# Kernel tuning notes

Hardware: AMD Instinct MI355X
Metric: run time of the kernel (lower is better)

The kernel has to match this reference:

```python
import jax, jax.numpy as jnp
import numpy as np
import math

N = 100000          # nodes
E = 3200000         # edges
F_IN = 500          # num_features
HID = 64            # hidden
C = 64              # num_classes
K = 5               # trig frequencies
OMEGA = 1.0
D = 10              # Taylor order / diffusion hops


def _taylor_coeffs():
    # cos/sin Taylor coefficient tables, [K, D+1] (static, fp64 then cast)
    x = (np.arange(1, K + 1) * OMEGA * np.pi)[:, None].astype(np.float64)
    cosc = np.zeros((K, D + 1), np.float64)
    sinc = np.zeros((K, D + 1), np.float64)
    even = np.arange(0, D + 1, 2)
    cosc[:, ::2] = ((-1.0) ** (even // 2)) * x ** even / np.array([math.factorial(int(o)) for o in even], np.float64)
    odd = np.arange(1, D + 1, 2)
    sinc[:, 1::2] = ((-1.0) ** ((odd - 1) // 2)) * x ** odd / np.array([math.factorial(int(o)) for o in odd], np.float64)
    return jnp.asarray(sinc, jnp.float32), jnp.asarray(cosc, jnp.float32)

SINC, COSC = _taylor_coeffs()


def setup_inputs() -> dict:
    key = jax.random.key(0)
    ks = jax.random.split(key, 8)
    feature = jax.random.normal(ks[0], (N, F_IN), dtype=jnp.float32)
    edges = jax.random.randint(ks[1], (2, E), 0, N, dtype=jnp.int64)
    W1 = jax.random.normal(ks[2], (F_IN, HID), dtype=jnp.float32) * (1.0 / np.sqrt(F_IN))
    b1 = jnp.zeros((HID,), jnp.float32)
    W2 = jax.random.normal(ks[3], (HID, C), dtype=jnp.float32) * (1.0 / np.sqrt(HID))
    b2 = jnp.zeros((C,), jnp.float32)
    xav = np.sqrt(2.0 / (1 + K))  # xavier_normal for (1, K)
    alpha = jax.random.normal(ks[4], (1, K), dtype=jnp.float32) * xav
    beta = jax.random.normal(ks[5], (1, K), dtype=jnp.float32) * xav
    return {"feature": feature, "edges": edges, "W1": W1, "b1": b1,
            "W2": W2, "b2": b2, "alpha": alpha, "beta": beta}


def reference(feature, edges, W1, b1, W2, b2, alpha, beta):
    # dropout is identity in eval mode
    x = jnp.maximum(feature @ W1 + b1, 0.0)   # lin1 + relu
    x = x @ W2 + b2                           # lin2 -> [N, C]

    # ---- Trigo_prop.__norm__: sym-normalized Laplacian, rescale, self-loops -1 ----
    src, dst = edges[0], edges[1]
    not_loop = src != dst                     # remove_self_loops
    deg = jax.ops.segment_sum(jnp.where(not_loop, 1.0, 0.0).astype(x.dtype), src, num_segments=N)
    dinv = jnp.where(deg > 0, jax.lax.rsqrt(deg), 0.0)
    w_off = jnp.where(not_loop, -(dinv[src] * dinv[dst]), 0.0)   # off-diag of L_sym
    # Laplacian diagonal entries are all 1 -> lambda_max = 2*max(all weights)
    lam = 2.0 * jnp.maximum(jnp.max(w_off), 1.0)
    s = 2.0 / lam
    w_off = w_off * s
    diag = s * 1.0 - 1.0                      # scaled diag(1) plus appended -1 self-loop

    # ---- D-hop Taylor-weighted diffusion ----
    coeff = (alpha @ SINC + beta @ COSC)[0]   # [D+1]
    Tx = x
    hidden = coeff[0] * Tx
    for d in range(1, D + 1):                 # fixed small D, unrolled
        Tx = jax.ops.segment_sum(w_off[:, None] * Tx[src], dst, num_segments=N) + diag * Tx
        hidden = hidden + coeff[d] * Tx
    out = hidden + x
    return jax.nn.log_softmax(out, axis=1)
```

## Files before the change

kernel.cpp:

```cpp
#include <hip/hip_runtime.h>
#include <math.h>

#define NN 100000
#define FIN 500
#define HIDN 64
#define KF 5
#define DORD 10
#define KPAD 512
#define NKT 8

typedef unsigned short ushort_t;
typedef __attribute__((ext_vector_type(8))) short short8v;
typedef __attribute__((ext_vector_type(4))) float f32x4;

struct Tables { float sinc[KF][DORD+1]; float cosc[KF][DORD+1]; };

__device__ inline float bl(unsigned u) { return __uint_as_float(u << 16); }
__device__ inline float bh(unsigned u) { return __uint_as_float(u & 0xffff0000u); }
__device__ inline unsigned short bf16_rne(float x) {
    unsigned u = __float_as_uint(x);
    return (unsigned short)((u + 0x7fffu + ((u >> 16) & 1u)) >> 16);
}
__device__ inline unsigned pack_bf16x2(float a, float b) {
    return (unsigned)bf16_rne(a) | ((unsigned)bf16_rne(b) << 16);
}

__global__ void coeff_kernel(const float* __restrict__ alpha, const float* __restrict__ beta,
                             Tables tb, float* __restrict__ coeff) {
    int d = threadIdx.x;
    if (d <= DORD) {
        float c = 0.f;
        #pragma unroll
        for (int k = 0; k < KF; ++k)
            c += alpha[k] * tb.sinc[k][d] + beta[k] * tb.cosc[k][d];
        coeff[d] = c;
    }
}

#define CHUNK 4096

__global__ __launch_bounds__(256) void hist_kernel(
    const int* __restrict__ src, const int* __restrict__ dst,
    int* __restrict__ histD, int* __restrict__ histS, int E, int nb) {
    __shared__ int hD[512];
    __shared__ int hS[512];
    for (int i = threadIdx.x; i < 512; i += 256) { hD[i] = 0; hS[i] = 0; }
    __syncthreads();
    int base = blockIdx.x * CHUNK;
    int end = base + CHUNK; if (end > E) end = E;
    for (int e = base + threadIdx.x; e < end; e += 256) {
        int s = src[e], d = dst[e];
        if (s != d) {
            atomicAdd(&hD[d >> 8], 1);
            atomicAdd(&hS[s >> 8], 1);
        }
    }
    __syncthreads();
    size_t ro = (size_t)blockIdx.x * 512;
    for (int i = threadIdx.x; i < nb; i += 256) {
        histD[ro + i] = hD[i];
        histS[ro + i] = hS[i];
    }
}

__global__ __launch_bounds__(512) void scanA_kernel(
    int* __restrict__ histD, int* __restrict__ histS,
    int* __restrict__ totD, int* __restrict__ totS, int nchunk, int nb) {
    __shared__ int tmp[512];
    int x = blockIdx.x;
    int* hist; int* tot; int b;
    if (x < nb) { hist = histD; tot = totD; b = x; }
    else        { hist = histS; tot = totS; b = x - nb; }
    int t = threadIdx.x;
    int carry = 0;
    for (int c0 = 0; c0 < nchunk; c0 += 512) {
        int c = c0 + t;
        tmp[t] = (c < nchunk) ? hist[(size_t)c * 512 + b] : 0;
        __syncthreads();
        for (int off = 1; off < 512; off <<= 1) {
            int add = (t >= off) ? tmp[t - off] : 0;
            __syncthreads();
            tmp[t] += add;
            __syncthreads();
        }
        if (c < nchunk) hist[(size_t)c * 512 + b] = carry + ((t > 0) ? tmp[t - 1] : 0);
        carry += tmp[511];
        __syncthreads();
    }
    if (t == 0) tot[b] = carry;
}

__global__ __launch_bounds__(512) void scanB_kernel(
    const int* __restrict__ totD, const int* __restrict__ totS,
    int* __restrict__ offD, int* __restrict__ offS, int nb) {
    __shared__ int tmp[512];
    int t = threadIdx.x;
    tmp[t] = (t < nb) ? totD[t] : 0;
    __syncthreads();
    for (int off = 1; off < 512; off <<= 1) {
        int add = (t >= off) ? tmp[t - off] : 0;
        __syncthreads();
        tmp[t] += add;
        __syncthreads();
    }
    if (t < nb) offD[t] = (t > 0) ? tmp[t - 1] : 0;
    if (t == nb - 1) offD[nb] = tmp[t];
    __syncthreads();
    tmp[t] = (t < nb) ? totS[t] : 0;
    __syncthreads();
    for (int off = 1; off < 512; off <<= 1) {
        int add = (t >= off) ? tmp[t - off] : 0;
        __syncthreads();
        tmp[t] += add;
        __syncthreads();
    }
    if (t < nb) offS[t] = (t > 0) ? tmp[t - 1] : 0;
    if (t == nb - 1) offS[nb] = tmp[t];
}

__global__ __launch_bounds__(256) void scatter_kernel(
    const int* __restrict__ src, const int* __restrict__ dst,
    const int* __restrict__ histD, const int* __restrict__ histS,
    const int* __restrict__ offD, const int* __restrict__ offS,
    unsigned* __restrict__ binned, unsigned char* __restrict__ srcbin, int E, int nb) {
    __shared__ int cD[512];
    __shared__ int cS[512];
    size_t ro = (size_t)blockIdx.x * 512;
    for (int i = threadIdx.x; i < nb; i += 256) {
        cD[i] = offD[i] + histD[ro + i];
        cS[i] = offS[i] + histS[ro + i];
    }
    __syncthreads();
    int base = blockIdx.x * CHUNK;
    int end = base + CHUNK; if (end > E) end = E;
    for (int e = base + threadIdx.x; e < end; e += 256) {
        int s = src[e], d = dst[e];
        if (s != d) {
            int pD = atomicAdd(&cD[d >> 8], 1);
            binned[pD] = (unsigned)s | ((unsigned)(d & 255) << 24);
            int pS = atomicAdd(&cS[s >> 8], 1);
            srcbin[pS] = (unsigned char)(s & 255);
        }
    }
}

__global__ __launch_bounds__(256) void bucket_csr_kernel(
    const unsigned* __restrict__ binned, const int* __restrict__ offD,
    int* __restrict__ row_ptr, int* __restrict__ col, int n, int nb) {
    int b = blockIdx.x;
    int e0 = offD[b], e1 = offD[b + 1];
    int d0 = b << 8;
    int dn = n - d0; if (dn > 256) dn = 256;
    __shared__ int ind[256];
    __shared__ int cur[256];
    int t = threadIdx.x;
    ind[t] = 0;
    __syncthreads();
    for (int e = e0 + t; e < e1; e += 256) {
        unsigned p = binned[e];
        atomicAdd(&ind[p >> 24], 1);
    }
    __syncthreads();
    for (int off = 1; off < 256; off <<= 1) {
        int add = (t >= off) ? ind[t - off] : 0;
        __syncthreads();
        ind[t] += add;
        __syncthreads();
    }
    if (t < dn) {
        int excl = (t > 0) ? ind[t - 1] : 0;
        row_ptr[d0 + t] = e0 + excl;
        cur[t] = e0 + excl;
    }
    if (b == 0 && t == 0) row_ptr[n] = offD[nb];
    __syncthreads();
    for (int e = e0 + t; e < e1; e += 256) {
        unsigned p = binned[e];
        int pos = atomicAdd(&cur[p >> 24], 1);
        col[pos] = (int)(p & 0xFFFFFFu);
    }
}

__global__ __launch_bounds__(256) void dinv_count_kernel(
    const unsigned char* __restrict__ srcbin, const int* __restrict__ offS,
    float* __restrict__ dinv, int n, int nb) {
    __shared__ int ind[256];
    int b = blockIdx.x;
    int t = threadIdx.x;
    ind[t] = 0;
    __syncthreads();
    int e0 = offS[b], e1 = offS[b + 1];
    for (int e = e0 + t; e < e1; e += 256)
        atomicAdd(&ind[srcbin[e]], 1);
    __syncthreads();
    int i = (b << 8) + t;
    if (i < n) {
        int c = ind[t];
        dinv[i] = (c > 0) ? (1.0f / sqrtf((float)c)) : 0.f;
    }
}

__global__ __launch_bounds__(256) void wprep_kernel(
    const float* __restrict__ W1, ushort_t* __restrict__ Wt) {
    int tid = blockIdx.x * 256 + threadIdx.x;
    if (tid >= 64 * KPAD) return;
    int kk = tid & (KPAD - 1);
    int c = tid >> 9;
    float v = (kk < FIN) ? W1[(size_t)kk * 64 + c] : 0.f;
    Wt[(size_t)c * KPAD + kk] = bf16_rne(v);
}

__global__ __launch_bounds__(256) void gemm1_mfma_kernel(
    const float* __restrict__ A, const ushort_t* __restrict__ Wt,
    const float* __restrict__ bias, float* __restrict__ H, int n) {
    __shared__ ushort_t sA[128][72];
    __shared__ ushort_t sB[64][72];
    int t = threadIdx.x;
    int w = t >> 6;
    int lane = t & 63;
    int lr = lane & 15;
    int lg = lane >> 4;
    int rowBase = blockIdx.x * 128;

    f32x4 acc[2][4];
    #pragma unroll
    for (int r = 0; r < 2; ++r)
        #pragma unroll
        for (int c = 0; c < 4; ++c)
            acc[r][c] = (f32x4){0.f, 0.f, 0.f, 0.f};

    for (int kt = 0; kt < NKT; ++kt) {
        #pragma unroll
        for (int l = 0; l < 8; ++l) {
            int idx = t + l * 256;
            int r = idx >> 4;
            int kc = (idx & 15) * 4;
            int gr = rowBase + r;
            int gk = kt * 64 + kc;
            float4 v = make_float4(0.f, 0.f, 0.f, 0.f);
            if (gr < n) {
                if (gk + 3 < FIN) {
                    v = *(const float4*)(A + (size_t)gr * FIN + gk);
                } else {
                    float* vp = (float*)&v;
                    #pragma unroll
                    for (int j = 0; j < 4; ++j)
                        if (gk + j < FIN) vp[j] = A[(size_t)gr * FIN + gk + j];
                }
            }
            uint2 p;
            p.x = pack_bf16x2(v.x, v.y);
            p.y = pack_bf16x2(v.z, v.w);
            *(uint2*)&sA[r][kc] = p;
        }
        #pragma unroll
        for (int l = 0; l < 2; ++l) {
            int idx = t + l * 256;
            int c = idx >> 3;
            int kc = (idx & 7) * 8;
            uint4 v = *(const uint4*)(Wt + (size_t)c * KPAD + kt * 64 + kc);
            *(uint4*)&sB[c][kc] = v;
        }
        __syncthreads();

        short8v af[2][2], bfr[4][2];
        #pragma unroll
        for (int r = 0; r < 2; ++r)
            #pragma unroll
            for (int h = 0; h < 2; ++h)
                af[r][h] = *(const short8v*)&sA[w * 32 + r * 16 + lr][h * 32 + lg * 8];
        #pragma unroll
        for (int c = 0; c < 4; ++c)
            #pragma unroll
            for (int h = 0; h < 2; ++h)
                bfr[c][h] = *(const short8v*)&sB[c * 16 + lr][h * 32 + lg * 8];
        #pragma unroll
        for (int r = 0; r < 2; ++r)
            #pragma unroll
            for (int c = 0; c < 4; ++c)
                #pragma unroll
                for (int h = 0; h < 2; ++h)
                    acc[r][c] = __builtin_amdgcn_mfma_f32_16x16x32_bf16(
                        af[r][h], bfr[c][h], acc[r][c], 0, 0, 0);
        __syncthreads();
    }

    float bcol[4];
    #pragma unroll
    for (int c = 0; c < 4; ++c) bcol[c] = bias[c * 16 + lr];
    #pragma unroll
    for (int r = 0; r < 2; ++r) {
        #pragma unroll
        for (int c = 0; c < 4; ++c) {
            #pragma unroll
            for (int i = 0; i < 4; ++i) {
                int row = rowBase + w * 32 + r * 16 + lg * 4 + i;
                if (row < n)
                    H[(size_t)row * 64 + c * 16 + lr] = fmaxf(acc[r][c][i] + bcol[c], 0.f);
            }
        }
    }
}

__global__ __launch_bounds__(256) void gemm2_kernel(
    const float* __restrict__ H, const float* __restrict__ W2,
    const float* __restrict__ b2, const float* __restrict__ coeff,
    const float* __restrict__ dinv, ushort_t* __restrict__ ty0,
    float* __restrict__ out, int n) {
    __shared__ float sW[64 * 64];
    __shared__ float sb[64];
    int t = threadIdx.x;
    for (int i = t; i < 4096; i += 256) sW[i] = W2[i];
    if (t < 64) sb[t] = b2[t];
    __syncthreads();
    float c0p1 = 1.f + coeff[0];
    int lane = t & 63;
    int wid = t >> 6;
    int r0 = blockIdx.x * 128;
    int rend = r0 + 128; if (rend > n) rend = n;
    for (int r = r0 + wid; r < rend; r += 4) {
        float hv = H[(size_t)r * 64 + lane];
        float dr = dinv[r];
        float acc = sb[lane];
        #pragma unroll
        for (int k = 0; k < 64; ++k)
            acc = fmaf(__shfl(hv, k, 64), sW[k * 64 + lane], acc);
        ty0[(size_t)r * 64 + lane] = bf16_rne(dr * acc);
        out[(size_t)r * 64 + lane] = c0p1 * acc;
    }
}

__global__ __launch_bounds__(256) void spmm_kernel(
    const int* __restrict__ row_ptr, const int* __restrict__ col,
    const float* __restrict__ dinv, const ushort_t* __restrict__ tyin,
    ushort_t* __restrict__ tyout, float* __restrict__ out,
    const float* __restrict__ coeff, int d, int n, int fuse_lsm) {
    int wave = (blockIdx.x * blockDim.x + threadIdx.x) >> 6;
    if (wave >= n) return;
    int lane = threadIdx.x & 63;
    int sub = lane >> 3;
    int fl = lane & 7;
    int e0 = row_ptr[wave], e1 = row_ptr[wave + 1];
    float a0 = 0.f, a1 = 0.f, a2 = 0.f, a3 = 0.f;
    float a4 = 0.f, a5 = 0.f, a6 = 0.f, a7 = 0.f;
    int e = e0 + sub;
    for (; e + 8 < e1; e += 16) {
        int s0 = col[e], s1 = col[e + 8];
        uint4 p0 = *(const uint4*)(tyin + (size_t)s0 * 64 + fl * 8);
        uint4 p1 = *(const uint4*)(tyin + (size_t)s1 * 64 + fl * 8);
        a0 += bl(p0.x) + bl(p1.x); a1 += bh(p0.x) + bh(p1.x);
        a2 += bl(p0.y) + bl(p1.y); a3 += bh(p0.y) + bh(p1.y);
        a4 += bl(p0.z) + bl(p1.z); a5 += bh(p0.z) + bh(p1.z);
        a6 += bl(p0.w) + bl(p1.w); a7 += bh(p0.w) + bh(p1.w);
    }
    if (e < e1) {
        int s = col[e];
        uint4 p = *(const uint4*)(tyin + (size_t)s * 64 + fl * 8);
        a0 += bl(p.x); a1 += bh(p.x); a2 += bl(p.y); a3 += bh(p.y);
        a4 += bl(p.z); a5 += bh(p.z); a6 += bl(p.w); a7 += bh(p.w);
    }
    #pragma unroll
    for (int off = 8; off <= 32; off <<= 1) {
        a0 += __shfl_xor(a0, off, 64); a1 += __shfl_xor(a1, off, 64);
        a2 += __shfl_xor(a2, off, 64); a3 += __shfl_xor(a3, off, 64);
        a4 += __shfl_xor(a4, off, 64); a5 += __shfl_xor(a5, off, 64);
        a6 += __shfl_xor(a6, off, 64); a7 += __shfl_xor(a7, off, 64);
    }
    float dr = dinv[wave];
    float cd = coeff[d];
    float t0 = -dr * a0, t1 = -dr * a1, t2 = -dr * a2, t3 = -dr * a3;
    float t4 = -dr * a4, t5 = -dr * a5, t6 = -dr * a6, t7 = -dr * a7;
    if (!fuse_lsm) {
        if (sub == 0) {
            float4 o0 = *(const float4*)(out + (size_t)wave * 64 + fl * 8);
            float4 o1 = *(const float4*)(out + (size_t)wave * 64 + fl * 8 + 4);
            o0.x += cd * t0; o0.y += cd * t1; o0.z += cd * t2; o0.w += cd * t3;
            o1.x += cd * t4; o1.y += cd * t5; o1.z += cd * t6; o1.w += cd * t7;
            *(float4*)(out + (size_t)wave * 64 + fl * 8) = o0;
            *(float4*)(out + (size_t)wave * 64 + fl * 8 + 4) = o1;
            uint4 ty;
            ty.x = pack_bf16x2(dr * t0, dr * t1);
            ty.y = pack_bf16x2(dr * t2, dr * t3);
            ty.z = pack_bf16x2(dr * t4, dr * t5);
            ty.w = pack_bf16x2(dr * t6, dr * t7);
            *(uint4*)(tyout + (size_t)wave * 64 + fl * 8) = ty;
        }
    } else {
        float4 o0 = *(const float4*)(out + (size_t)wave * 64 + fl * 8);
        float4 o1 = *(const float4*)(out + (size_t)wave * 64 + fl * 8 + 4);
        o0.x += cd * t0; o0.y += cd * t1; o0.z += cd * t2; o0.w += cd * t3;
        o1.x += cd * t4; o1.y += cd * t5; o1.z += cd * t6; o1.w += cd * t7;
        float m = fmaxf(fmaxf(fmaxf(o0.x, o0.y), fmaxf(o0.z, o0.w)),
                        fmaxf(fmaxf(o1.x, o1.y), fmaxf(o1.z, o1.w)));
        #pragma unroll
        for (int off = 1; off < 8; off <<= 1) m = fmaxf(m, __shfl_xor(m, off, 64));
        float se = expf(o0.x - m) + expf(o0.y - m) + expf(o0.z - m) + expf(o0.w - m)
                 + expf(o1.x - m) + expf(o1.y - m) + expf(o1.z - m) + expf(o1.w - m);
        #pragma unroll
        for (int off = 1; off < 8; off <<= 1) se += __shfl_xor(se, off, 64);
        float lse = m + logf(se);
        o0.x -= lse; o0.y -= lse; o0.z -= lse; o0.w -= lse;
        o1.x -= lse; o1.y -= lse; o1.z -= lse; o1.w -= lse;
        if (sub == 0) {
            *(float4*)(out + (size_t)wave * 64 + fl * 8) = o0;
            *(float4*)(out + (size_t)wave * 64 + fl * 8 + 4) = o1;
        }
    }
}

extern "C" void kernel_launch(void* const* d_in, const int* in_sizes, int n_in,
                              void* d_out, int out_size, void* d_ws, size_t ws_size,
                              hipStream_t stream) {
    const float* feature = (const float*)d_in[0];
    const int*   edges   = (const int*)d_in[1];
    const float* W1      = (const float*)d_in[2];
    const float* b1      = (const float*)d_in[3];
    const float* W2      = (const float*)d_in[4];
    const float* b2      = (const float*)d_in[5];
    const float* alpha   = (const float*)d_in[6];
    const float* beta    = (const float*)d_in[7];
    float* out = (float*)d_out;

    const int n = in_sizes[0] / FIN;
    const int E = in_sizes[1] / 2;
    const int* src = edges;
    const int* dst = edges + E;

    const int nb = (n + 255) >> 8;
    const int nchunk = (E + CHUNK - 1) / CHUNK;
    const size_t n64 = (size_t)n * 64;

    char* ws = (char*)d_ws;
    size_t off = 0;
    auto alloc = [&](size_t bytes) { size_t o = off; off = (off + bytes + 255) & ~(size_t)255; return o; };
    float*         coeff   = (float*)        (ws + alloc(64 * 4));
    float*         dinv    = (float*)        (ws + alloc((size_t)n * 4));
    int*           row_ptr = (int*)          (ws + alloc(((size_t)n + 1) * 4));
    int*           offD    = (int*)          (ws + alloc(513 * 4));
    int*           offS    = (int*)          (ws + alloc(513 * 4));
    int*           totD    = (int*)          (ws + alloc(512 * 4));
    int*           totS    = (int*)          (ws + alloc(512 * 4));
    ushort_t*      Wt      = (ushort_t*)     (ws + alloc((size_t)64 * KPAD * 2));
    int*           histD   = (int*)          (ws + alloc((size_t)nchunk * 512 * 4));
    int*           histS   = (int*)          (ws + alloc((size_t)nchunk * 512 * 4));
    int*           col     = (int*)          (ws + alloc((size_t)E * 4));
    unsigned*      binned  = (unsigned*)     (ws + alloc((size_t)E * 4));
    unsigned char* srcbin  = (unsigned char*)(ws + alloc((size_t)E));
    float*         H       = (float*)        (ws + alloc(n64 * 4));
    ushort_t*      TyA     = (ushort_t*)     (ws + alloc(n64 * 2));
    ushort_t*      TyB     = (ushort_t*)     (ws + alloc(n64 * 2));

    Tables tb;
    for (int k = 0; k < KF; ++k) {
        double x = M_PI * (double)(k + 1);
        double p = 1.0, f = 1.0;
        for (int o = 0; o <= DORD; ++o) {
            if (o > 0) { p *= x; f *= (double)o; }
            double v = p / f;
            tb.cosc[k][o] = (o % 2 == 0) ? (float)((((o / 2) % 2 == 0) ? 1.0 : -1.0) * v) : 0.f;
            tb.sinc[k][o] = (o % 2 == 1) ? (float)(((((o - 1) / 2) % 2 == 0) ? 1.0 : -1.0) * v) : 0.f;
        }
    }

    coeff_kernel<<<1, 64, 0, stream>>>(alpha, beta, tb, coeff);
    wprep_kernel<<<(64 * KPAD + 255) / 256, 256, 0, stream>>>(W1, Wt);

    hist_kernel<<<nchunk, 256, 0, stream>>>(src, dst, histD, histS, E, nb);
    scanA_kernel<<<2 * nb, 512, 0, stream>>>(histD, histS, totD, totS, nchunk, nb);
    scanB_kernel<<<1, 512, 0, stream>>>(totD, totS, offD, offS, nb);
    scatter_kernel<<<nchunk, 256, 0, stream>>>(src, dst, histD, histS, offD, offS,
                                               binned, srcbin, E, nb);
    bucket_csr_kernel<<<nb, 256, 0, stream>>>(binned, offD, row_ptr, col, n, nb);
    dinv_count_kernel<<<nb, 256, 0, stream>>>(srcbin, offS, dinv, n, nb);

    gemm1_mfma_kernel<<<(n + 127) / 128, 256, 0, stream>>>(feature, Wt, b1, H, n);
    gemm2_kernel<<<(n + 127) / 128, 256, 0, stream>>>(H, W2, b2, coeff, dinv, TyA, out, n);

    const ushort_t* tin = TyA;
    ushort_t* bufs[2] = { TyB, TyA };
    for (int d = 1; d <= DORD; ++d) {
        ushort_t* tout = bufs[(d - 1) & 1];
        spmm_kernel<<<(n + 3) / 4, 256, 0, stream>>>(row_ptr, col, dinv, tin, tout, out,
                                                     coeff, d, n, d == DORD ? 1 : 0);
        tin = tout;
    }
}
```

Before: 1.181 ms.

## Fuse ten SpMM diffusion hops into one persistent kernel with grid barriers

Replaces the ten per-hop SpMM launches with a single persistent kernel of 1536 blocks. Each wave owns a fixed range of rows and keeps their output accumulators in shared memory across hops, with hops separated by a software grid barrier built on atomics. This removes launch gaps and the per-hop read-modify-write of the fp32 output in global memory. In exchange it relies on all blocks being co-resident to avoid deadlock, and it loses dynamic load balancing because each wave processes up to 17 rows serially. If 17 × 6144 waves were fewer than n, rows would be silently skipped, though that does not happen for n=100000.

```diff
diff --git a/kernel.cpp b/kernel.cpp
--- a/kernel.cpp
+++ b/kernel.cpp
@@ -8,6 +8,8 @@
 #define DORD 10
 #define KPAD 512
 #define NKT 8
+#define FUSE_GRID 1536
+#define RPW_MAX 17
 
 typedef unsigned short ushort_t;
 typedef __attribute__((ext_vector_type(8))) short short8v;
@@ -330,81 +332,104 @@
     }
 }
 
-__global__ __launch_bounds__(256) void spmm_kernel(
+__device__ __forceinline__ void grid_bar(int* cnt, int* flag, int nblk) {
+    __syncthreads();
+    if (threadIdx.x == 0) {
+        __threadfence();
+        int old = __hip_atomic_fetch_add(cnt, 1, __ATOMIC_ACQ_REL, __HIP_MEMORY_SCOPE_AGENT);
+        if (old == nblk - 1) {
+            __hip_atomic_store(flag, 1, __ATOMIC_RELEASE, __HIP_MEMORY_SCOPE_AGENT);
+        } else {
+            while (__hip_atomic_load(flag, __ATOMIC_RELAXED, __HIP_MEMORY_SCOPE_AGENT) == 0)
+                __builtin_amdgcn_s_sleep(8);
+        }
+        __threadfence();
+    }
+    __syncthreads();
+}
+
+__global__ __launch_bounds__(256, 6) void diffuse_kernel(
     const int* __restrict__ row_ptr, const int* __restrict__ col,
-    const float* __restrict__ dinv, const ushort_t* __restrict__ tyin,
-    ushort_t* __restrict__ tyout, float* __restrict__ out,
-    const float* __restrict__ coeff, int d, int n, int fuse_lsm) {
-    int wave = (blockIdx.x * blockDim.x + threadIdx.x) >> 6;
-    if (wave >= n) return;
-    int lane = threadIdx.x & 63;
+    const float* __restrict__ dinv, const float* __restrict__ coeff,
+    ushort_t* TyA, ushort_t* TyB,
+    float* out, int* bars, int n) {
+    __shared__ float oacc[4][RPW_MAX][64];
+    int t = threadIdx.x;
+    int w = t >> 6, lane = t & 63;
     int sub = lane >> 3;
     int fl = lane & 7;
-    int e0 = row_ptr[wave], e1 = row_ptr[wave + 1];
-    float a0 = 0.f, a1 = 0.f, a2 = 0.f, a3 = 0.f;
-    float a4 = 0.f, a5 = 0.f, a6 = 0.f, a7 = 0.f;
-    int e = e0 + sub;
-    for (; e + 8 < e1; e += 16) {
-        int s0 = col[e], s1 = col[e + 8];
-        uint4 p0 = *(const uint4*)(tyin + (size_t)s0 * 64 + fl * 8);
-        uint4 p1 = *(const uint4*)(tyin + (size_t)s1 * 64 + fl * 8);
-        a0 += bl(p0.x) + bl(p1.x); a1 += bh(p0.x) + bh(p1.x);
-        a2 += bl(p0.y) + bl(p1.y); a3 += bh(p0.y) + bh(p1.y);
-        a4 += bl(p0.z) + bl(p1.z); a5 += bh(p0.z) + bh(p1.z);
-        a6 += bl(p0.w) + bl(p1.w); a7 += bh(p0.w) + bh(p1.w);
-    }
-    if (e < e1) {
-        int s = col[e];
-        uint4 p = *(const uint4*)(tyin + (size_t)s * 64 + fl * 8);
-        a0 += bl(p.x); a1 += bh(p.x); a2 += bl(p.y); a3 += bh(p.y);
-        a4 += bl(p.z); a5 += bh(p.z); a6 += bl(p.w); a7 += bh(p.w);
-    }
-    #pragma unroll
-    for (int off = 8; off <= 32; off <<= 1) {
-        a0 += __shfl_xor(a0, off, 64); a1 += __shfl_xor(a1, off, 64);
-        a2 += __shfl_xor(a2, off, 64); a3 += __shfl_xor(a3, off, 64);
-        a4 += __shfl_xor(a4, off, 64); a5 += __shfl_xor(a5, off, 64);
-        a6 += __shfl_xor(a6, off, 64); a7 += __shfl_xor(a7, off, 64);
-    }
-    float dr = dinv[wave];
-    float cd = coeff[d];
-    float t0 = -dr * a0, t1 = -dr * a1, t2 = -dr * a2, t3 = -dr * a3;
-    float t4 = -dr * a4, t5 = -dr * a5, t6 = -dr * a6, t7 = -dr * a7;
-    if (!fuse_lsm) {
-        if (sub == 0) {
-            float4 o0 = *(const float4*)(out + (size_t)wave * 64 + fl * 8);
-            float4 o1 = *(const float4*)(out + (size_t)wave * 64 + fl * 8 + 4);
-            o0.x += cd * t0; o0.y += cd * t1; o0.z += cd * t2; o0.w += cd * t3;
-            o1.x += cd * t4; o1.y += cd * t5; o1.z += cd * t6; o1.w += cd * t7;
-            *(float4*)(out + (size_t)wave * 64 + fl * 8) = o0;
-            *(float4*)(out + (size_t)wave * 64 + fl * 8 + 4) = o1;
-            uint4 ty;
-            ty.x = pack_bf16x2(dr * t0, dr * t1);
-            ty.y = pack_bf16x2(dr * t2, dr * t3);
-            ty.z = pack_bf16x2(dr * t4, dr * t5);
-            ty.w = pack_bf16x2(dr * t6, dr * t7);
-            *(uint4*)(tyout + (size_t)wave * 64 + fl * 8) = ty;
-        }
-    } else {
-        float4 o0 = *(const float4*)(out + (size_t)wave * 64 + fl * 8);
-        float4 o1 = *(const float4*)(out + (size_t)wave * 64 + fl * 8 + 4);
-        o0.x += cd * t0; o0.y += cd * t1; o0.z += cd * t2; o0.w += cd * t3;
-        o1.x += cd * t4; o1.y += cd * t5; o1.z += cd * t6; o1.w += cd * t7;
-        float m = fmaxf(fmaxf(fmaxf(o0.x, o0.y), fmaxf(o0.z, o0.w)),
-                        fmaxf(fmaxf(o1.x, o1.y), fmaxf(o1.z, o1.w)));
-        #pragma unroll
-        for (int off = 1; off < 8; off <<= 1) m = fmaxf(m, __shfl_xor(m, off, 64));
-        float se = expf(o0.x - m) + expf(o0.y - m) + expf(o0.z - m) + expf(o0.w - m)
-                 + expf(o1.x - m) + expf(o1.y - m) + expf(o1.z - m) + expf(o1.w - m);
-        #pragma unroll
-        for (int off = 1; off < 8; off <<= 1) se += __shfl_xor(se, off, 64);
-        float lse = m + logf(se);
-        o0.x -= lse; o0.y -= lse; o0.z -= lse; o0.w -= lse;
-        o1.x -= lse; o1.y -= lse; o1.z -= lse; o1.w -= lse;
-        if (sub == 0) {
-            *(float4*)(out + (size_t)wave * 64 + fl * 8) = o0;
-            *(float4*)(out + (size_t)wave * 64 + fl * 8 + 4) = o1;
-        }
+    int nblk = gridDim.x;
+    int nw = nblk * 4;
+    int rpw = (n + nw - 1) / nw;
+    if (rpw > RPW_MAX) rpw = RPW_MAX;
+    int gid = blockIdx.x * 4 + w;
+    int r0 = gid * rpw;
+    int r1 = r0 + rpw; if (r1 > n) r1 = n;
+    int fmap = fl * 8 + sub;
+
+    for (int r = r0; r < r1; ++r)
+        oacc[w][r - r0][lane] = out[(size_t)r * 64 + fmap];
+
+    for (int d = 1; d <= DORD; ++d) {
+        const ushort_t* tin = ((d - 1) & 1) ? TyB : TyA;
+        ushort_t* tout = (d & 1) ? TyB : TyA;
+        float cd = coeff[d];
+        for (int r = r0; r < r1; ++r) {
+            int e0 = row_ptr[r], e1 = row_ptr[r + 1];
+            float a0 = 0.f, a1 = 0.f, a2 = 0.f, a3 = 0.f;
+            float a4 = 0.f, a5 = 0.f, a6 = 0.f, a7 = 0.f;
+            int e = e0 + sub;
+            for (; e + 8 < e1; e += 16) {
+                int s0 = col[e], s1 = col[e + 8];
+                uint4 p0 = *(const uint4*)(tin + (size_t)s0 * 64 + fl * 8);
+                uint4 p1 = *(const uint4*)(tin + (size_t)s1 * 64 + fl * 8);
+                a0 += bl(p0.x) + bl(p1.x); a1 += bh(p0.x) + bh(p1.x);
+                a2 += bl(p0.y) + bl(p1.y); a3 += bh(p0.y) + bh(p1.y);
+                a4 += bl(p0.z) + bl(p1.z); a5 += bh(p0.z) + bh(p1.z);
+                a6 += bl(p0.w) + bl(p1.w); a7 += bh(p0.w) + bh(p1.w);
+            }
+            if (e < e1) {
+                int s = col[e];
+                uint4 p = *(const uint4*)(tin + (size_t)s * 64 + fl * 8);
+                a0 += bl(p.x); a1 += bh(p.x); a2 += bl(p.y); a3 += bh(p.y);
+                a4 += bl(p.z); a5 += bh(p.z); a6 += bl(p.w); a7 += bh(p.w);
+            }
+            #pragma unroll
+            for (int off = 8; off <= 32; off <<= 1) {
+                a0 += __shfl_xor(a0, off, 64); a1 += __shfl_xor(a1, off, 64);
+                a2 += __shfl_xor(a2, off, 64); a3 += __shfl_xor(a3, off, 64);
+                a4 += __shfl_xor(a4, off, 64); a5 += __shfl_xor(a5, off, 64);
+                a6 += __shfl_xor(a6, off, 64); a7 += __shfl_xor(a7, off, 64);
+            }
+            float dr = dinv[r];
+            float t0 = -dr * a0, t1 = -dr * a1, t2 = -dr * a2, t3 = -dr * a3;
+            float t4 = -dr * a4, t5 = -dr * a5, t6 = -dr * a6, t7 = -dr * a7;
+            if (d < DORD && sub == 0) {
+                uint4 ty;
+                ty.x = pack_bf16x2(dr * t0, dr * t1);
+                ty.y = pack_bf16x2(dr * t2, dr * t3);
+                ty.z = pack_bf16x2(dr * t4, dr * t5);
+                ty.w = pack_bf16x2(dr * t6, dr * t7);
+                *(uint4*)(tout + (size_t)r * 64 + fl * 8) = ty;
+            }
+            float tj = (sub < 4) ? ((sub < 2) ? (sub == 0 ? t0 : t1) : (sub == 2 ? t2 : t3))
+                                 : ((sub < 6) ? (sub == 4 ? t4 : t5) : (sub == 6 ? t6 : t7));
+            oacc[w][r - r0][lane] += cd * tj;
+        }
+        if (d < DORD)
+            grid_bar(&bars[2 * d], &bars[2 * d + 1], nblk);
+    }
+
+    for (int r = r0; r < r1; ++r) {
+        float v = oacc[w][r - r0][lane];
+        float m = v;
+        #pragma unroll
+        for (int off = 1; off < 64; off <<= 1) m = fmaxf(m, __shfl_xor(m, off, 64));
+        float s = expf(v - m);
+        #pragma unroll
+        for (int off = 1; off < 64; off <<= 1) s += __shfl_xor(s, off, 64);
+        float lse = m + logf(s);
+        out[(size_t)r * 64 + fmap] = v - lse;
     }
 }
 
@@ -434,6 +459,7 @@
     size_t off = 0;
     auto alloc = [&](size_t bytes) { size_t o = off; off = (off + bytes + 255) & ~(size_t)255; return o; };
     float*         coeff   = (float*)        (ws + alloc(64 * 4));
+    int*           bars    = (int*)          (ws + alloc(64 * 4));
     float*         dinv    = (float*)        (ws + alloc((size_t)n * 4));
     int*           row_ptr = (int*)          (ws + alloc(((size_t)n + 1) * 4));
     int*           offD    = (int*)          (ws + alloc(513 * 4));
@@ -462,6 +488,7 @@
         }
     }
 
+    hipMemsetAsync(bars, 0, 64 * 4, stream);
     coeff_kernel<<<1, 64, 0, stream>>>(alpha, beta, tb, coeff);
     wprep_kernel<<<(64 * KPAD + 255) / 256, 256, 0, stream>>>(W1, Wt);
 
@@ -476,12 +503,6 @@
     gemm1_mfma_kernel<<<(n + 127) / 128, 256, 0, stream>>>(feature, Wt, b1, H, n);
     gemm2_kernel<<<(n + 127) / 128, 256, 0, stream>>>(H, W2, b2, coeff, dinv, TyA, out, n);
 
-    const ushort_t* tin = TyA;
-    ushort_t* bufs[2] = { TyB, TyA };
-    for (int d = 1; d <= DORD; ++d) {
-        ushort_t* tout = bufs[(d - 1) & 1];
-        spmm_kernel<<<(n + 3) / 4, 256, 0, stream>>>(row_ptr, col, dinv, tin, tout, out,
-                                                     coeff, d, n, d == DORD ? 1 : 0);
-        tin = tout;
-    }
-}
+    diffuse_kernel<<<FUSE_GRID, 256, 0, stream>>>(row_ptr, col, dinv, coeff,
+                                                  TyA, TyB, out, bars, n);
+}
```

After: 3.483 ms. +194.9%, slower.

## Fuse second linear layer into MFMA GEMM1 and unroll SpMM gather by four

Applied to the files above, without the earlier changes.

Fuses the lin2 matmul into the first MFMA GEMM kernel. The ReLU hidden tile is written to shared memory as bf16, then multiplied by a pre-transposed bf16 W2 with MFMA. This removes the fp32 H intermediate round trip through global memory and one kernel launch. Separately, the SpMM gather loop gets a four-edge unrolled stage so more loads are in flight. The tradeoff is bf16 rounding of the hidden activations before lin2, plus extra LDS use.

```diff
diff --git a/kernel.cpp b/kernel.cpp
--- a/kernel.cpp
+++ b/kernel.cpp
@@ -201,26 +201,45 @@
 }
 
 __global__ __launch_bounds__(256) void wprep_kernel(
-    const float* __restrict__ W1, ushort_t* __restrict__ Wt) {
+    const float* __restrict__ W1, const float* __restrict__ W2,
+    ushort_t* __restrict__ Wt, ushort_t* __restrict__ W2t) {
     int tid = blockIdx.x * 256 + threadIdx.x;
-    if (tid >= 64 * KPAD) return;
-    int kk = tid & (KPAD - 1);
-    int c = tid >> 9;
-    float v = (kk < FIN) ? W1[(size_t)kk * 64 + c] : 0.f;
-    Wt[(size_t)c * KPAD + kk] = bf16_rne(v);
-}
-
-__global__ __launch_bounds__(256) void gemm1_mfma_kernel(
+    if (tid < 64 * KPAD) {
+        int kk = tid & (KPAD - 1);
+        int c = tid >> 9;
+        float v = (kk < FIN) ? W1[(size_t)kk * 64 + c] : 0.f;
+        Wt[(size_t)c * KPAD + kk] = bf16_rne(v);
+    } else if (tid < 64 * KPAD + 64 * 64) {
+        int j = tid - 64 * KPAD;
+        int kk = j & 63;
+        int c = j >> 6;
+        W2t[(size_t)c * 64 + kk] = bf16_rne(W2[(size_t)kk * 64 + c]);
+    }
+}
+
+__global__ __launch_bounds__(256) void gemm12_kernel(
     const float* __restrict__ A, const ushort_t* __restrict__ Wt,
-    const float* __restrict__ bias, float* __restrict__ H, int n) {
+    const ushort_t* __restrict__ W2t,
+    const float* __restrict__ b1, const float* __restrict__ b2,
+    const float* __restrict__ coeff, const float* __restrict__ dinv,
+    ushort_t* __restrict__ ty0, float* __restrict__ out, int n) {
     __shared__ ushort_t sA[128][72];
     __shared__ ushort_t sB[64][72];
+    __shared__ ushort_t sB2[64][72];
     int t = threadIdx.x;
     int w = t >> 6;
     int lane = t & 63;
     int lr = lane & 15;
     int lg = lane >> 4;
     int rowBase = blockIdx.x * 128;
+
+    #pragma unroll
+    for (int l = 0; l < 2; ++l) {
+        int idx = t + l * 256;
+        int c = idx >> 3, kc = (idx & 7) * 8;
+        uint4 v = *(const uint4*)(W2t + (size_t)c * 64 + kc);
+        *(uint4*)&sB2[c][kc] = v;
+    }
 
     f32x4 acc[2][4];
     #pragma unroll
@@ -285,48 +304,64 @@
         __syncthreads();
     }
 
-    float bcol[4];
-    #pragma unroll
-    for (int c = 0; c < 4; ++c) bcol[c] = bias[c * 16 + lr];
+    float bcol1[4];
+    #pragma unroll
+    for (int c = 0; c < 4; ++c) bcol1[c] = b1[c * 16 + lr];
+    #pragma unroll
+    for (int r = 0; r < 2; ++r)
+        #pragma unroll
+        for (int c = 0; c < 4; ++c)
+            #pragma unroll
+            for (int i = 0; i < 4; ++i)
+                sA[w * 32 + r * 16 + lg * 4 + i][c * 16 + lr] =
+                    bf16_rne(fmaxf(acc[r][c][i] + bcol1[c], 0.f));
+    __syncthreads();
+
+    short8v af2[2][2], bf2[4][2];
+    #pragma unroll
+    for (int r = 0; r < 2; ++r)
+        #pragma unroll
+        for (int h = 0; h < 2; ++h)
+            af2[r][h] = *(const short8v*)&sA[w * 32 + r * 16 + lr][h * 32 + lg * 8];
+    #pragma unroll
+    for (int c = 0; c < 4; ++c)
+        #pragma unroll
+        for (int h = 0; h < 2; ++h)
+            bf2[c][h] = *(const short8v*)&sB2[c * 16 + lr][h * 32 + lg * 8];
+    f32x4 acc2[2][4];
+    #pragma unroll
+    for (int r = 0; r < 2; ++r)
+        #pragma unroll
+        for (int c = 0; c < 4; ++c)
+            acc2[r][c] = (f32x4){0.f, 0.f, 0.f, 0.f};
+    #pragma unroll
+    for (int r = 0; r < 2; ++r)
+        #pragma unroll
+        for (int c = 0; c < 4; ++c)
+            #pragma unroll
+            for (int h = 0; h < 2; ++h)
+                acc2[r][c] = __builtin_amdgcn_mfma_f32_16x16x32_bf16(
+                    af2[r][h], bf2[c][h], acc2[r][c], 0, 0, 0);
+
+    float c0p1 = 1.f + coeff[0];
+    float bcol2[4];
+    #pragma unroll
+    for (int c = 0; c < 4; ++c) bcol2[c] = b2[c * 16 + lr];
     #pragma unroll
     for (int r = 0; r < 2; ++r) {
         #pragma unroll
-        for (int c = 0; c < 4; ++c) {
-            #pragma unroll
-            for (int i = 0; i < 4; ++i) {
-                int row = rowBase + w * 32 + r * 16 + lg * 4 + i;
-                if (row < n)
-                    H[(size_t)row * 64 + c * 16 + lr] = fmaxf(acc[r][c][i] + bcol[c], 0.f);
+        for (int i = 0; i < 4; ++i) {
+            int row = rowBase + w * 32 + r * 16 + lg * 4 + i;
+            if (row < n) {
+                float dr = dinv[row];
+                #pragma unroll
+                for (int c = 0; c < 4; ++c) {
+                    float X = acc2[r][c][i] + bcol2[c];
+                    out[(size_t)row * 64 + c * 16 + lr] = c0p1 * X;
+                    ty0[(size_t)row * 64 + c * 16 + lr] = bf16_rne(dr * X);
+                }
             }
         }
-    }
-}
-
-__global__ __launch_bounds__(256) void gemm2_kernel(
-    const float* __restrict__ H, const float* __restrict__ W2,
-    const float* __restrict__ b2, const float* __restrict__ coeff,
-    const float* __restrict__ dinv, ushort_t* __restrict__ ty0,
-    float* __restrict__ out, int n) {
-    __shared__ float sW[64 * 64];
-    __shared__ float sb[64];
-    int t = threadIdx.x;
-    for (int i = t; i < 4096; i += 256) sW[i] = W2[i];
-    if (t < 64) sb[t] = b2[t];
-    __syncthreads();
-    float c0p1 = 1.f + coeff[0];
-    int lane = t & 63;
-    int wid = t >> 6;
-    int r0 = blockIdx.x * 128;
-    int rend = r0 + 128; if (rend > n) rend = n;
-    for (int r = r0 + wid; r < rend; r += 4) {
-        float hv = H[(size_t)r * 64 + lane];
-        float dr = dinv[r];
-        float acc = sb[lane];
-        #pragma unroll
-        for (int k = 0; k < 64; ++k)
-            acc = fmaf(__shfl(hv, k, 64), sW[k * 64 + lane], acc);
-        ty0[(size_t)r * 64 + lane] = bf16_rne(dr * acc);
-        out[(size_t)r * 64 + lane] = c0p1 * acc;
     }
 }
 
@@ -344,6 +379,21 @@
     float a0 = 0.f, a1 = 0.f, a2 = 0.f, a3 = 0.f;
     float a4 = 0.f, a5 = 0.f, a6 = 0.f, a7 = 0.f;
     int e = e0 + sub;
+    for (; e + 24 < e1; e += 32) {
+        int s0 = col[e], s1 = col[e + 8], s2 = col[e + 16], s3 = col[e + 24];
+        uint4 p0 = *(const uint4*)(tyin + (size_t)s0 * 64 + fl * 8);
+        uint4 p1 = *(const uint4*)(tyin + (size_t)s1 * 64 + fl * 8);
+        uint4 p2 = *(const uint4*)(tyin + (size_t)s2 * 64 + fl * 8);
+        uint4 p3 = *(const uint4*)(tyin + (size_t)s3 * 64 + fl * 8);
+        a0 += (bl(p0.x) + bl(p1.x)) + (bl(p2.x) + bl(p3.x));
+        a1 += (bh(p0.x) + bh(p1.x)) + (bh(p2.x) + bh(p3.x));
+        a2 += (bl(p0.y) + bl(p1.y)) + (bl(p2.y) + bl(p3.y));
+        a3 += (bh(p0.y) + bh(p1.y)) + (bh(p2.y) + bh(p3.y));
+        a4 += (bl(p0.z) + bl(p1.z)) + (bl(p2.z) + bl(p3.z));
+        a5 += (bh(p0.z) + bh(p1.z)) + (bh(p2.z) + bh(p3.z));
+        a6 += (bl(p0.w) + bl(p1.w)) + (bl(p2.w) + bl(p3.w));
+        a7 += (bh(p0.w) + bh(p1.w)) + (bh(p2.w) + bh(p3.w));
+    }
     for (; e + 8 < e1; e += 16) {
         int s0 = col[e], s1 = col[e + 8];
         uint4 p0 = *(const uint4*)(tyin + (size_t)s0 * 64 + fl * 8);
@@ -441,12 +491,12 @@
     int*           totD    = (int*)          (ws + alloc(512 * 4));
     int*           totS    = (int*)          (ws + alloc(512 * 4));
     ushort_t*      Wt      = (ushort_t*)     (ws + alloc((size_t)64 * KPAD * 2));
+    ushort_t*      W2t     = (ushort_t*)     (ws + alloc((size_t)64 * 64 * 2));
     int*           histD   = (int*)          (ws + alloc((size_t)nchunk * 512 * 4));
     int*           histS   = (int*)          (ws + alloc((size_t)nchunk * 512 * 4));
     int*           col     = (int*)          (ws + alloc((size_t)E * 4));
     unsigned*      binned  = (unsigned*)     (ws + alloc((size_t)E * 4));
     unsigned char* srcbin  = (unsigned char*)(ws + alloc((size_t)E));
-    float*         H       = (float*)        (ws + alloc(n64 * 4));
     ushort_t*      TyA     = (ushort_t*)     (ws + alloc(n64 * 2));
     ushort_t*      TyB     = (ushort_t*)     (ws + alloc(n64 * 2));
 
@@ -463,7 +513,7 @@
     }
 
     coeff_kernel<<<1, 64, 0, stream>>>(alpha, beta, tb, coeff);
-    wprep_kernel<<<(64 * KPAD + 255) / 256, 256, 0, stream>>>(W1, Wt);
+    wprep_kernel<<<(64 * KPAD + 64 * 64 + 255) / 256, 256, 0, stream>>>(W1, W2, Wt, W2t);
 
     hist_kernel<<<nchunk, 256, 0, stream>>>(src, dst, histD, histS, E, nb);
     scanA_kernel<<<2 * nb, 512, 0, stream>>>(histD, histS, totD, totS, nchunk, nb);
@@ -473,8 +523,8 @@
     bucket_csr_kernel<<<nb, 256, 0, stream>>>(binned, offD, row_ptr, col, n, nb);
     dinv_count_kernel<<<nb, 256, 0, stream>>>(srcbin, offS, dinv, n, nb);
 
-    gemm1_mfma_kernel<<<(n + 127) / 128, 256, 0, stream>>>(feature, Wt, b1, H, n);
-    gemm2_kernel<<<(n + 127) / 128, 256, 0, stream>>>(H, W2, b2, coeff, dinv, TyA, out, n);
+    gemm12_kernel<<<(n + 127) / 128, 256, 0, stream>>>(feature, Wt, W2t, b1, b2,
+                                                       coeff, dinv, TyA, out, n);
 
     const ushort_t* tin = TyA;
     ushort_t* bufs[2] = { TyB, TyA };
```

Result: faster. 1.097 ms (-7.2%).
